# Kernel tuning notes

Hardware: AMD Instinct MI355X
Metric: run time of the kernel (lower is better)

The kernel has to match this reference:

```python
import jax, jax.numpy as jnp
import numpy as np

N, HIDDEN, K = 16384, 256, 5  # k=5 neighbors, first (self) dropped -> 4 hyperedge memberships per node


def _knn_hyperedges(x):
    # Mimics sklearn NearestNeighbors(k=5) + drop self (torch code detaches x here).
    xs = jax.lax.stop_gradient(x)
    n = xs.shape[0]
    sq = jnp.sum(xs * xs, axis=1)
    d2 = sq[:, None] + sq[None, :] - 2.0 * (xs @ xs.T)  # [N, N] squared distances
    d2 = d2.at[jnp.arange(n), jnp.arange(n)].set(jnp.inf)  # exclude self
    _, idx = jax.lax.top_k(-d2, K - 1)  # [N, K-1] nearest neighbors
    node_idx = jnp.repeat(jnp.arange(n), K - 1)  # hyperedge_index[0]: node i
    edge_idx = idx.reshape(-1)                   # hyperedge_index[1]: hyperedge id = neighbor id
    return node_idx, edge_idx


def _prelu(x, a):
    return jnp.where(x >= 0, x, a * x)


def _hconv(x, W, b, node_idx, edge_idx, n):
    # PyG HypergraphConv (heads=1, no attention, unit hyperedge weights):
    # out = D^{-1} H B^{-1} H^T (x W^T) + b
    xt = x @ W.T  # lin has no bias in PyG; bias added at the end
    ones = jnp.ones(node_idx.shape[0], dtype=x.dtype)
    Bdeg = jax.ops.segment_sum(ones, edge_idx, num_segments=n)  # hyperedge degree
    Binv = jnp.where(Bdeg > 0, 1.0 / Bdeg, 0.0)
    Ddeg = jax.ops.segment_sum(ones, node_idx, num_segments=n)  # node degree
    Dinv = jnp.where(Ddeg > 0, 1.0 / Ddeg, 0.0)
    # node -> hyperedge gather/scatter
    e_feat = jax.ops.segment_sum(xt[node_idx], edge_idx, num_segments=n) * Binv[:, None]
    # hyperedge -> node gather/scatter
    out = jax.ops.segment_sum(e_feat[edge_idx], node_idx, num_segments=n) * Dinv[:, None]
    return out + b


def setup_inputs() -> dict:
    key = jax.random.key(0)
    k0, k1, k2, k3 = jax.random.split(key, 4)
    x = jax.random.normal(k0, (N, HIDDEN), dtype=jnp.float32)
    edge_index = jax.random.randint(k1, (2, 65536), 0, N)  # unused by the math, kept per signature
    kaiming = np.sqrt(2.0 / HIDDEN)
    W1 = jax.random.normal(k2, (HIDDEN, HIDDEN), dtype=jnp.float32) * kaiming
    W2 = jax.random.normal(k3, (HIDDEN, HIDDEN), dtype=jnp.float32) * kaiming
    b1 = jnp.zeros((HIDDEN,), dtype=jnp.float32)
    b2 = jnp.zeros((HIDDEN,), dtype=jnp.float32)
    prelu_a = jnp.float32(0.25)  # nn.PReLU() default single shared parameter
    return {"x": x, "edge_index": edge_index, "W1": W1, "b1": b1, "W2": W2, "b2": b2, "prelu_a": prelu_a}


def reference(x, edge_index, W1, b1, W2, b2, prelu_a):
    n = x.shape[0]
    node_idx, edge_idx = _knn_hyperedges(x)
    h = _hconv(x, W1, b1, node_idx, edge_idx, n)
    h = _prelu(h, prelu_a)
    h = _hconv(h, W2, b2, node_idx, edge_idx, n)
    h = h + x  # residual
    return _prelu(h, prelu_a)
```

## Files before the change

### kernel.cpp

```cpp
#include <hip/hip_runtime.h>
#include <stdint.h>

#define NN   16384
#define HID  256
#define LDSK 264
#define NSLICE 16
#define JSL  (NN/NSLICE)
#define JT   32
#define NIT  (JSL/JT)
#define NSETS 4
#define ITILE (NSETS*64)
#define NRS  8
#define GSB  2048
#define NWV  (GSB*4)
#define FLTMAX 3.402823466e38f
#define KEYMAX 0xFFFFFFFFu
#define VBIAS 131072.0f
#define MSTRIDE 17

typedef __attribute__((ext_vector_type(8))) _Float16 f16x8;
typedef __attribute__((ext_vector_type(4))) _Float16 f16x4;
typedef __attribute__((ext_vector_type(4))) float f32x4;

typedef const __attribute__((address_space(1))) unsigned int* gAS1;
typedef __attribute__((address_space(3))) unsigned int* lAS3;

#define NXG (NN*HID/4)
#define NWG (HID*HID/4)
#define CVTB ((NXG + 2*NWG)/256)
__global__ __launch_bounds__(256) void prep_kernel(const float* __restrict__ x,
                                                   const float* __restrict__ W1,
                                                   const float* __restrict__ W2,
                                                   _Float16* __restrict__ xh,
                                                   _Float16* __restrict__ W1h,
                                                   _Float16* __restrict__ W2h,
                                                   float* __restrict__ sqf,
                                                   int* __restrict__ Bdeg){
  #pragma clang fp contract(off)
  int b = blockIdx.x;
  int g0 = b * 256 + threadIdx.x;
  if (g0 < NN) Bdeg[g0] = 0;
  if (b < CVTB){
    int g = g0;
    const float* src; _Float16* dst; int o;
    if (g < NXG)            { src = x;  dst = xh;  o = g; }
    else if (g < NXG + NWG) { src = W1; dst = W1h; o = g - NXG; }
    else                    { src = W2; dst = W2h; o = g - NXG - NWG; }
    float4 v = ((const float4*)src)[o];
    f16x4 h; h.x = (_Float16)v.x; h.y = (_Float16)v.y; h.z = (_Float16)v.z; h.w = (_Float16)v.w;
    ((f16x4*)dst)[o] = h;
  } else {
    int bb = b - CVTB;
    int lane = threadIdx.x & 63;
    int rw   = lane >> 4;
    int h    = (lane >> 3) & 1;
    int j    = lane & 7;
    int row  = (bb * 4 + (threadIdx.x >> 6)) * 4 + rw;
    const float* p = x + (size_t)row * HID + h*128 + j;
    float v0 = p[0];
    float r  = v0 * v0;
    #pragma unroll
    for (int i = 1; i < 16; ++i){ float v = p[i*8]; float m = v * v; r = r + m; }
    float t1 = r  + __shfl_xor(r,  1);
    float t2 = t1 + __shfl_xor(t1, 2);
    float t3 = t2 + __shfl_xor(t2, 4);
    float tot = t3 + __shfl_xor(t3, 8);
    if (h == 0 && j == 0) sqf[row] = tot;
  }
}

__device__ __forceinline__ void load_tile64(unsigned short* dst, const unsigned short* src, int tid){
  const uint4* s = (const uint4*)src;
  #pragma unroll
  for (int r = 0; r < 8; ++r){
    int fl  = tid + (r << 8);
    int row = fl >> 5;
    int c   = fl & 31;
    *(uint4*)&dst[row*LDSK + (c << 3)] = s[fl];
  }
}

__device__ __forceinline__ unsigned umed3(unsigned a, unsigned b, unsigned c){
  unsigned d;
  asm("v_med3_u32 %0, %1, %2, %3" : "=v"(d) : "v"(a), "v"(b), "v"(c));
  return d;
}
__device__ __forceinline__ void ins4(unsigned (&b)[4], unsigned k){
  unsigned b0 = b[0], b1 = b[1], b2 = b[2];
  b[0] = k < b0 ? k : b0;
  b[1] = umed3(k, b0, b1);
  b[2] = umed3(k, b1, b2);
  b[3] = umed3(k, b2, b[3]);
}

__global__ __launch_bounds__(256, 2) void knn_kernel(const _Float16* __restrict__ xh,
                                                     const float* __restrict__ sqf,
                                                     unsigned* __restrict__ candk){
  __shared__ __align__(16) unsigned short Xj[2][JT*256];
  __shared__ __align__(16) float sqjA[JSL];

  int tid  = threadIdx.x;
  int sl   = blockIdx.x & (NSLICE-1);
  int i0   = (blockIdx.x / NSLICE) * ITILE;
  int jb0  = sl * JSL;
  int wave = tid >> 6, lane = tid & 63, quad = lane >> 4, lcol = lane & 15;

  f16x8 bfr[NSETS][8];
  #pragma unroll
  for (int s = 0; s < NSETS; ++s){
    const _Float16* br = xh + (size_t)(i0 + s*64 + wave*16 + lcol) * HID + quad*8;
    #pragma unroll
    for (int ks = 0; ks < 8; ++ks) bfr[s][ks] = *(const f16x8*)(br + ks*32);
  }

  const _Float16* gsrc[4];
  #pragma unroll
  for (int r = 0; r < 4; ++r){
    int m   = r*256 + tid;
    int row = m >> 5;
    int ch  = m & 31;
    gsrc[r] = xh + (size_t)row * HID + ((ch ^ (row & 7)) << 3);
  }

  int b0 = lcol*512 + ((quad ^ (lcol & 3)) << 4) + (((lcol >> 2) & 1) << 6);
  int b1 = b0 ^ 64;

  unsigned bk[NSETS][4];
  #pragma unroll
  for (int s = 0; s < NSETS; ++s)
    #pragma unroll
    for (int e = 0; e < 4; ++e) bk[s][e] = KEYMAX;

  {
    float4 sv = ((const float4*)(sqf + jb0))[tid];
    float4 sw;
    sw.x = fmaf(sv.x, 64.f, VBIAS); sw.y = fmaf(sv.y, 64.f, VBIAS);
    sw.z = fmaf(sv.z, 64.f, VBIAS); sw.w = fmaf(sv.w, 64.f, VBIAS);
    ((float4*)sqjA)[tid] = sw;
    size_t joff = (size_t)jb0 * HID;
    #pragma unroll
    for (int r = 0; r < 4; ++r)
      __builtin_amdgcn_global_load_lds((gAS1)(const void*)(gsrc[r] + joff),
                                       (lAS3)(void*)&Xj[0][(r*256 + tid) * 8],
                                       16, 0, 0);
    asm volatile("s_waitcnt vmcnt(0) lgkmcnt(0)" ::: "memory");
  }
  __builtin_amdgcn_s_barrier();
  __builtin_amdgcn_sched_barrier(0);

  for (int it = 0; it < NIT; ++it){
    int cur = it & 1;
    if (it + 1 < NIT){
      int nb = cur ^ 1;
      int jn = jb0 + (it + 1) * JT;
      size_t joff = (size_t)jn * HID;
      #pragma unroll
      for (int r = 0; r < 4; ++r)
        __builtin_amdgcn_global_load_lds((gAS1)(const void*)(gsrc[r] + joff),
                                         (lAS3)(void*)&Xj[nb][(r*256 + tid) * 8],
                                         16, 0, 0);
      asm volatile("s_waitcnt vmcnt(4)" ::: "memory");
    } else {
      asm volatile("s_waitcnt vmcnt(0)" ::: "memory");
    }
    __builtin_amdgcn_s_barrier();
    __builtin_amdgcn_sched_barrier(0);

    const char*  tb  = (const char*)&Xj[cur][0];
    const float* sjb = &sqjA[it * JT];
    int jb = jb0 + it * JT;

    #pragma unroll
    for (int sub = 0; sub < 2; ++sub){
      f32x4 acc[NSETS];
      #pragma unroll
      for (int s = 0; s < NSETS; ++s) acc[s] = (f32x4){0.f,0.f,0.f,0.f};
      #pragma unroll
      for (int ks = 0; ks < 8; ++ks){
        f16x8 a = *(const f16x8*)(tb + sub*8192 + ((ks >> 1) << 7) + ((ks & 1) ? b1 : b0));
        #pragma unroll
        for (int s = 0; s < NSETS; ++s)
          acc[s] = __builtin_amdgcn_mfma_f32_16x16x32_f16(a, bfr[s][ks], acc[s], 0, 0, 0);
      }
      float4 sj4 = *(const float4*)&sjb[sub*16 + quad*4];
      int jbase = jb + sub*16 + quad*4;
      #pragma unroll
      for (int reg = 0; reg < 4; ++reg){
        int gj = jbase + reg;
        float sj = (&sj4.x)[reg];
        #pragma unroll
        for (int s = 0; s < NSETS; ++s){
          float v64 = fmaf(-128.f, acc[s][reg], sj);
          unsigned kv = (unsigned)v64;
          unsigned key = (kv << 14) + (unsigned)gj;
          ins4(bk[s], key);
        }
      }
    }
    asm volatile("s_waitcnt lgkmcnt(0)" ::: "memory");
    __builtin_amdgcn_s_barrier();
    __builtin_amdgcn_sched_barrier(0);
  }

  unsigned* Mk = (unsigned*)Xj;
  #pragma unroll
  for (int s = 0; s < NSETS; ++s){
    int base = (s*64 + wave*16 + lcol)*MSTRIDE + quad*4;
    #pragma unroll
    for (int e = 0; e < 4; ++e) Mk[base+e] = bk[s][e];
  }
  __syncthreads();
  if (tid < ITILE){
    unsigned fk[4];
    #pragma unroll
    for (int e = 0; e < 4; ++e) fk[e] = KEYMAX;
    #pragma unroll
    for (int s = 0; s < 16; ++s) ins4(fk, Mk[tid*MSTRIDE + s]);
    int g = i0 + tid;
    #pragma unroll
    for (int e = 0; e < 4; ++e)
      candk[(size_t)g*(NSLICE*4) + sl*4 + e] = fk[e];
  }
}

__global__ __launch_bounds__(64) void rescore_kernel(const float* __restrict__ x,
                                                     const float* __restrict__ sqf,
                                                     const unsigned* __restrict__ candk,
                                                     int* __restrict__ idx_out,
                                                     int* __restrict__ Bdeg){
  #pragma clang fp contract(off)
  __shared__ float Xi[256];
  __shared__ float Xct[256][NRS+1];
  __shared__ float dex[NRS];
  __shared__ int   sel[NRS];
  int i = blockIdx.x;
  int t = threadIdx.x;
  ((float4*)Xi)[t] = ((const float4*)(x + (size_t)i * HID))[t];
  unsigned kv = candk[(size_t)i*(NSLICE*4) + t];
  if ((kv & 16383u) == (unsigned)i) kv = KEYMAX;
  int rank = 0;
  for (int s = 0; s < 64; ++s){
    unsigned ks = __shfl(kv, s);
    rank += (ks < kv) ? 1 : 0;
  }
  if (rank < NRS) sel[rank] = (int)(kv & 16383u);
  __syncthreads();
  {
    int r = t >> 3, seg = t & 7;
    const float4* src = (const float4*)(x + (size_t)sel[r] * HID);
    #pragma unroll
    for (int m = 0; m < 8; ++m){
      float4 v = src[seg + 8*m];
      int k = 4*(seg + 8*m);
      Xct[k+0][r] = v.x; Xct[k+1][r] = v.y; Xct[k+2][r] = v.z; Xct[k+3][r] = v.w;
    }
  }
  __syncthreads();
  if (t < NRS){
    int j = sel[t];
    float acc = 0.f;
    for (int k = 0; k < 256; ++k) acc = fmaf(Xi[k], Xct[k][t], acc);
    float t1   = sqf[i] + sqf[j];
    float twod = 2.0f * acc;
    dex[t] = t1 - twod;
  }
  __syncthreads();
  if (t == 0){
    unsigned taken = 0;
    #pragma unroll
    for (int k = 0; k < 4; ++k){
      float bdv = FLTMAX; int bj = 0x7fffffff, bs = -1;
      for (int s = 0; s < NRS; ++s){
        if (taken & (1u << s)) continue;
        float d = dex[s]; int j = sel[s];
        if (d < bdv || (d == bdv && j < bj)){ bdv = d; bj = j; bs = s; }
      }
      taken |= 1u << bs;
      idx_out[i*4 + k] = bj;
      atomicAdd(&Bdeg[bj], 1);
    }
  }
}

__global__ __launch_bounds__(256) void gemm_xw(const _Float16* __restrict__ A,
                                               const _Float16* __restrict__ W,
                                               _Float16* __restrict__ out){
  __shared__ unsigned short Ws[64 * LDSK];
  int tid = threadIdx.x;
  int i0 = (blockIdx.x >> 2) * 64;
  int o0 = (blockIdx.x & 3)  * 64;
  int wave = tid >> 6, lane = tid & 63, quad = lane >> 4, lcol = lane & 15;
  load_tile64(Ws, (const unsigned short*)(W + (size_t)o0 * HID), tid);
  f16x8 a[8];
  const _Float16* arow = A + (size_t)(i0 + wave*16 + lcol) * HID + quad*8;
  #pragma unroll
  for (int ks = 0; ks < 8; ++ks) a[ks] = *(const f16x8*)(arow + ks*32);
  __syncthreads();
  #pragma unroll
  for (int sub = 0; sub < 4; ++sub){
    f32x4 acc = {0.f, 0.f, 0.f, 0.f};
    #pragma unroll
    for (int ks = 0; ks < 8; ++ks){
      f16x8 b = *(const f16x8*)&Ws[(sub*16 + lcol)*LDSK + quad*8 + ks*32];
      acc = __builtin_amdgcn_mfma_f32_16x16x32_f16(a[ks], b, acc, 0, 0, 0);
    }
    #pragma unroll
    for (int reg = 0; reg < 4; ++reg)
      out[(size_t)(i0 + wave*16 + quad*4 + reg)*HID + o0 + sub*16 + lcol] = (_Float16)acc[reg];
  }
}

__global__ __launch_bounds__(256) void prefix_kernel(const int* __restrict__ Bdeg,
                                                     int* __restrict__ off,
                                                     int* __restrict__ cursor){
  __shared__ int psum[256];
  __shared__ int excl[256];
  int t = threadIdx.x;
  int base = t * 64;
  int s = 0;
  for (int k = 0; k < 64; ++k) s += Bdeg[base + k];
  psum[t] = s;
  __syncthreads();
  if (t == 0){ int a = 0; for (int k = 0; k < 256; ++k){ excl[k] = a; a += psum[k]; } }
  __syncthreads();
  int a = excl[t];
  for (int k = 0; k < 64; ++k){ int dv = Bdeg[base + k]; off[base+k] = a; cursor[base+k] = a; a += dv; }
}

__global__ __launch_bounds__(256) void fill_kernel(const int* __restrict__ idx,
                                                   int* __restrict__ cursor,
                                                   int* __restrict__ rev){
  int i = blockIdx.x * 256 + threadIdx.x;
  #pragma unroll
  for (int t = 0; t < 4; ++t){
    int e = idx[i*4 + t];
    int p = atomicAdd(&cursor[e], 1);
    rev[p] = i;
  }
}

__global__ __launch_bounds__(256) void efeat_kernel(const _Float16* __restrict__ xt,
                                                    const int* __restrict__ off,
                                                    const int* __restrict__ deg,
                                                    const int* __restrict__ rev,
                                                    _Float16* __restrict__ E){
  int wv   = blockIdx.x * 4 + (threadIdx.x >> 6);
  int lane = threadIdx.x & 63;
  for (int e = wv; e < NN; e += NWV){
    int o = off[e], d = deg[e];
    float s0 = 0.f, s1 = 0.f, s2 = 0.f, s3 = 0.f;
    #pragma unroll 4
    for (int k = 0; k < d; ++k){
      int node = rev[o + k];
      f16x4 v = *(const f16x4*)(xt + (size_t)node * HID + lane * 4);
      s0 += (float)v.x; s1 += (float)v.y; s2 += (float)v.z; s3 += (float)v.w;
    }
    f16x4 w;
    if (d > 0){
      float fd = (float)d;
      w.x = (_Float16)(s0 / fd); w.y = (_Float16)(s1 / fd);
      w.z = (_Float16)(s2 / fd); w.w = (_Float16)(s3 / fd);
    } else {
      w.x = (_Float16)0.f; w.y = (_Float16)0.f; w.z = (_Float16)0.f; w.w = (_Float16)0.f;
    }
    *(f16x4*)(E + (size_t)e * HID + lane * 4) = w;
  }
}

__global__ __launch_bounds__(256) void fin1_kernel(const _Float16* __restrict__ E,
                                                   const int* __restrict__ idx,
                                                   const float* __restrict__ b1,
                                                   const float* __restrict__ pa,
                                                   _Float16* __restrict__ h1){
  int wv   = blockIdx.x * 4 + (threadIdx.x >> 6);
  int lane = threadIdx.x & 63;
  float4 bc = ((const float4*)b1)[lane];
  float a   = pa[0];
  for (int i = wv; i < NN; i += NWV){
    const int* ip = idx + i*4;
    int e0 = ip[0], e1 = ip[1], e2 = ip[2], e3 = ip[3];
    f16x4 v0 = *(const f16x4*)(E + (size_t)e0*HID + lane*4);
    f16x4 v1 = *(const f16x4*)(E + (size_t)e1*HID + lane*4);
    f16x4 v2 = *(const f16x4*)(E + (size_t)e2*HID + lane*4);
    f16x4 v3 = *(const f16x4*)(E + (size_t)e3*HID + lane*4);
    f16x4 w;
    #pragma unroll
    for (int c = 0; c < 4; ++c){
      float s = ((float)v0[c] + (float)v1[c] + (float)v2[c] + (float)v3[c]);
      float acc = 0.25f * s + (&bc.x)[c];
      acc = (acc >= 0.f) ? acc : a * acc;
      w[c] = (_Float16)acc;
    }
    *(f16x4*)(h1 + (size_t)i*HID + lane*4) = w;
  }
}

__global__ __launch_bounds__(256) void fin2_kernel(const _Float16* __restrict__ E,
                                                   const int* __restrict__ idx,
                                                   const float* __restrict__ b2,
                                                   const float* __restrict__ x,
                                                   const float* __restrict__ pa,
                                                   float* __restrict__ out){
  int wv   = blockIdx.x * 4 + (threadIdx.x >> 6);
  int lane = threadIdx.x & 63;
  float4 bc = ((const float4*)b2)[lane];
  float a   = pa[0];
  for (int i = wv; i < NN; i += NWV){
    const int* ip = idx + i*4;
    int e0 = ip[0], e1 = ip[1], e2 = ip[2], e3 = ip[3];
    f16x4 v0 = *(const f16x4*)(E + (size_t)e0*HID + lane*4);
    f16x4 v1 = *(const f16x4*)(E + (size_t)e1*HID + lane*4);
    f16x4 v2 = *(const f16x4*)(E + (size_t)e2*HID + lane*4);
    f16x4 v3 = *(const f16x4*)(E + (size_t)e3*HID + lane*4);
    float4 xr = *(const float4*)(x + (size_t)i*HID + lane*4);
    float4 w;
    #pragma unroll
    for (int c = 0; c < 4; ++c){
      float s = ((float)v0[c] + (float)v1[c] + (float)v2[c] + (float)v3[c]);
      float acc = 0.25f * s + (&bc.x)[c] + (&xr.x)[c];
      acc = (acc >= 0.f) ? acc : a * acc;
      (&w.x)[c] = acc;
    }
    *(float4*)(out + (size_t)i*HID + lane*4) = w;
  }
}

extern "C" void kernel_launch(void* const* d_in, const int* in_sizes, int n_in,
                              void* d_out, int out_size, void* d_ws, size_t ws_size,
                              hipStream_t stream){
  (void)in_sizes; (void)n_in; (void)out_size; (void)ws_size;
  const float* x  = (const float*)d_in[0];
  const float* W1 = (const float*)d_in[2];
  const float* b1 = (const float*)d_in[3];
  const float* W2 = (const float*)d_in[4];
  const float* b2 = (const float*)d_in[5];
  const float* pa = (const float*)d_in[6];
  float* out = (float*)d_out;

  char* ws = (char*)d_ws;
  float*  sqf    = (float*) (ws + 0);
  int*    idx    = (int*)   (ws + 65536);
  int*    Bdeg   = (int*)   (ws + 327680);
  int*    offE   = (int*)   (ws + 393216);
  int*    cursor = (int*)   (ws + 458752);
  int*    rev    = (int*)   (ws + 524288);
  _Float16* xh   = (_Float16*)(ws + (size_t)(5<<20));
  _Float16* W1h  = (_Float16*)(ws + (size_t)(13<<20));
  _Float16* W2h  = (_Float16*)(ws + (size_t)(13<<20) + 131072);
  _Float16* xt   = (_Float16*)(ws + (size_t)(13<<20) + 262144);
  _Float16* E    = (_Float16*)(ws + (size_t)(21<<20) + 262144);
  _Float16* h1   = (_Float16*)(ws + (size_t)(29<<20) + 262144);
  unsigned* candk = (unsigned*)xt;

  prep_kernel   <<<CVTB + NN/16, 256, 0, stream>>>(x, W1, W2, xh, W1h, W2h, sqf, Bdeg);
  knn_kernel    <<<(NN/ITILE)*NSLICE, 256, 0, stream>>>(xh, sqf, candk);
  rescore_kernel<<<NN, 64, 0, stream>>>(x, sqf, candk, idx, Bdeg);
  prefix_kernel <<<1, 256, 0, stream>>>(Bdeg, offE, cursor);
  fill_kernel   <<<NN/256, 256, 0, stream>>>(idx, cursor, rev);

  gemm_xw       <<<(NN/64)*4, 256, 0, stream>>>(xh, W1h, xt);
  efeat_kernel  <<<GSB, 256, 0, stream>>>(xt, offE, Bdeg, rev, E);
  fin1_kernel   <<<GSB, 256, 0, stream>>>(E, idx, b1, pa, h1);

  gemm_xw       <<<(NN/64)*4, 256, 0, stream>>>(h1, W2h, xt);
  efeat_kernel  <<<GSB, 256, 0, stream>>>(xt, offE, Bdeg, rev, E);
  fin2_kernel   <<<GSB, 256, 0, stream>>>(E, idx, b2, x, pa, out);
}
```

Before: 437.0 us.

## Rescore eight nodes per block with per-thread candidate dot products

The rescore kernel now handles eight query nodes per 64-thread block instead of one. Each thread ranks eight candidate keys through shared memory, and each of the 64 threads then computes one exact fp32 distance directly from global memory. Previously only eight threads did the dot products after an LDS transpose. This cuts the block count eightfold and removes the serial single-wave dot product, at the cost of uncoalesced per-thread row reads from global memory.

```diff
diff --git a/kernel.cpp b/kernel.cpp
--- a/kernel.cpp
+++ b/kernel.cpp
@@ -229,54 +229,71 @@
                                                      int* __restrict__ idx_out,
                                                      int* __restrict__ Bdeg){
   #pragma clang fp contract(off)
-  __shared__ float Xi[256];
-  __shared__ float Xct[256][NRS+1];
-  __shared__ float dex[NRS];
-  __shared__ int   sel[NRS];
-  int i = blockIdx.x;
+  __shared__ unsigned Mk[8][65];
+  __shared__ int   sel[8][8];
+  __shared__ float dex[8][8];
   int t = threadIdx.x;
-  ((float4*)Xi)[t] = ((const float4*)(x + (size_t)i * HID))[t];
-  unsigned kv = candk[(size_t)i*(NSLICE*4) + t];
-  if ((kv & 16383u) == (unsigned)i) kv = KEYMAX;
-  int rank = 0;
+  int n = t >> 3, c = t & 7;
+  int g = blockIdx.x * 8 + n;
+
+  unsigned kr[8];
+  {
+    const uint4* kp = (const uint4*)(candk + (size_t)g*64 + c*8);
+    uint4 k0 = kp[0], k1 = kp[1];
+    kr[0]=k0.x; kr[1]=k0.y; kr[2]=k0.z; kr[3]=k0.w;
+    kr[4]=k1.x; kr[5]=k1.y; kr[6]=k1.z; kr[7]=k1.w;
+  }
+  #pragma unroll
+  for (int q = 0; q < 8; ++q)
+    if ((kr[q] & 16383u) == (unsigned)g) kr[q] = KEYMAX;
+  #pragma unroll
+  for (int q = 0; q < 8; ++q) Mk[n][c*8+q] = kr[q];
+  __syncthreads();
+
+  int rank[8];
+  #pragma unroll
+  for (int q = 0; q < 8; ++q) rank[q] = 0;
   for (int s = 0; s < 64; ++s){
-    unsigned ks = __shfl(kv, s);
-    rank += (ks < kv) ? 1 : 0;
-  }
-  if (rank < NRS) sel[rank] = (int)(kv & 16383u);
-  __syncthreads();
+    unsigned ks = Mk[n][s];
+    #pragma unroll
+    for (int q = 0; q < 8; ++q) rank[q] += (ks < kr[q]) ? 1 : 0;
+  }
+  #pragma unroll
+  for (int q = 0; q < 8; ++q)
+    if (rank[q] < NRS) sel[n][rank[q]] = (int)(kr[q] & 16383u);
+  __syncthreads();
+
   {
-    int r = t >> 3, seg = t & 7;
-    const float4* src = (const float4*)(x + (size_t)sel[r] * HID);
-    #pragma unroll
-    for (int m = 0; m < 8; ++m){
-      float4 v = src[seg + 8*m];
-      int k = 4*(seg + 8*m);
-      Xct[k+0][r] = v.x; Xct[k+1][r] = v.y; Xct[k+2][r] = v.z; Xct[k+3][r] = v.w;
-    }
-  }
-  __syncthreads();
-  if (t < NRS){
-    int j = sel[t];
+    int j = sel[n][c];
+    const float4* xi = (const float4*)(x + (size_t)g * HID);
+    const float4* xj = (const float4*)(x + (size_t)j * HID);
     float acc = 0.f;
-    for (int k = 0; k < 256; ++k) acc = fmaf(Xi[k], Xct[k][t], acc);
-    float t1   = sqf[i] + sqf[j];
+    for (int k4 = 0; k4 < HID/4; ++k4){
+      float4 a = xi[k4];
+      float4 b = xj[k4];
+      acc = fmaf(a.x, b.x, acc);
+      acc = fmaf(a.y, b.y, acc);
+      acc = fmaf(a.z, b.z, acc);
+      acc = fmaf(a.w, b.w, acc);
+    }
+    float t1   = sqf[g] + sqf[j];
     float twod = 2.0f * acc;
-    dex[t] = t1 - twod;
-  }
-  __syncthreads();
-  if (t == 0){
+    dex[n][c] = t1 - twod;
+  }
+  __syncthreads();
+
+  if (c == 0){
     unsigned taken = 0;
     #pragma unroll
     for (int k = 0; k < 4; ++k){
       float bdv = FLTMAX; int bj = 0x7fffffff, bs = -1;
       for (int s = 0; s < NRS; ++s){
         if (taken & (1u << s)) continue;
-        float d = dex[s]; int j = sel[s];
+        float d = dex[n][s]; int j = sel[n][s];
         if (d < bdv || (d == bdv && j < bj)){ bdv = d; bj = j; bs = s; }
       }
       taken |= 1u << bs;
-      idx_out[i*4 + k] = bj;
+      idx_out[g*4 + k] = bj;
       atomicAdd(&Bdeg[bj], 1);
     }
   }
@@ -454,7 +471,7 @@
 
   prep_kernel   <<<CVTB + NN/16, 256, 0, stream>>>(x, W1, W2, xh, W1h, W2h, sqf, Bdeg);
   knn_kernel    <<<(NN/ITILE)*NSLICE, 256, 0, stream>>>(xh, sqf, candk);
-  rescore_kernel<<<NN, 64, 0, stream>>>(x, sqf, candk, idx, Bdeg);
+  rescore_kernel<<<NN/8, 64, 0, stream>>>(x, sqf, candk, idx, Bdeg);
   prefix_kernel <<<1, 256, 0, stream>>>(Bdeg, offE, cursor);
   fill_kernel   <<<NN/256, 256, 0, stream>>>(idx, cursor, rev);
 
```

Result: faster. 421.9 us (-3.5%).
